# Performance work log

Hardware: AMD Instinct MI355X
Metric: run time of the kernel (lower is better)

## Reference

```python
import jax, jax.numpy as jnp
import numpy as np

# ROUTER_CONFIG constants
TOP_K = 2
EXPLORATION_BONUS = 0.1
EMA_ALPHA = 0.99
B, D, E, O, CTX = 16384, 256, 8, 128, 32


def setup_inputs() -> dict:
    key = jax.random.key(0)
    ks = jax.random.split(key, 16)
    s = 0.05  # small init scale to avoid tanh saturation
    return {
        "x": jax.random.normal(ks[0], (B, D), jnp.float32),
        "targets": jax.random.normal(ks[1], (B, O), jnp.float32),
        "W1": jax.random.normal(ks[2], (D, 64), jnp.float32) * s,
        "b1": jnp.zeros((64,), jnp.float32),
        "W2": jax.random.normal(ks[3], (64, CTX), jnp.float32) * s,
        "b2": jnp.zeros((CTX,), jnp.float32),
        "S1": jax.random.normal(ks[4], (CTX, 32), jnp.float32) * s,
        "sb1": jnp.zeros((32,), jnp.float32),
        "S2": jax.random.normal(ks[5], (32, E), jnp.float32) * s,
        "sb2": jnp.zeros((E,), jnp.float32),
        "We": jax.random.normal(ks[6], (E, D, O), jnp.float32) * s,
        "be": jnp.zeros((E, O), jnp.float32),
        "expert_rewards": jax.random.normal(ks[7], (E,), jnp.float32),
        "routing_ema": jnp.ones((E,), jnp.float32) / E,
        "expert_pulls": jax.random.randint(ks[8], (E,), 0, 500, jnp.int32),
        "total_selections": 1000,
    }


def reference(x, targets, W1, b1, W2, b2, S1, sb1, S2, sb2, We, be,
              expert_rewards, routing_ema, expert_pulls, total_selections):
    # --- context encoder (dropout inactive / eval) ---
    h = jax.nn.relu(x @ W1 + b1)
    context = jnp.tanh(h @ W2 + b2)                      # [B, CTX]
    # --- expert scorer ---
    scores = jax.nn.relu(context @ S1 + sb1) @ S2 + sb2  # [B, E]
    # --- UCB terms ---
    pulls_f = expert_pulls.astype(jnp.float32)
    safe_pulls = jnp.clip(pulls_f, 1.0, None)
    explo = EXPLORATION_BONUS * jnp.sqrt(
        jnp.log(jnp.float32(total_selections)) / safe_pulls)   # [E]
    avg_reward = jnp.where(pulls_f > 0, expert_rewards / safe_pulls, 0.0)
    ucb = scores + avg_reward[None, :] + explo[None, :]   # [B, E]
    # --- top-k selection + routing weights ---
    top_vals, top_idx = jax.lax.top_k(ucb, TOP_K)         # [B, k]
    routing_w = jax.nn.softmax(top_vals, axis=1)          # [B, k]
    # --- expert forward (all experts, then gather selected) ---
    all_out = jnp.einsum('bd,edo->beo', x, We) + be       # [B, E, O]
    sel_out = jnp.take_along_axis(all_out, top_idx[:, :, None], axis=1)  # [B,k,O]
    predictions = jnp.einsum('bk,bko->bo', routing_w, sel_out)           # [B,O]
    # --- per-expert MSE losses -> rewards ---
    losses = jnp.mean((sel_out - targets[:, None, :]) ** 2, axis=-1)  # [B,k]
    rewards = -losses
    # --- vectorized bandit stat updates (replaces python loops) ---
    flat_idx = top_idx.reshape(-1)
    counts = jax.ops.segment_sum(jnp.ones_like(rewards).reshape(-1), flat_idx, num_segments=E)
    rsum = jax.ops.segment_sum(rewards.reshape(-1), flat_idx, num_segments=E)
    new_pulls = pulls_f + counts
    new_total_rewards = expert_rewards + rsum
    new_avg_reward = jnp.where(new_pulls > 0, new_total_rewards / jnp.clip(new_pulls, 1.0, None), 0.0)
    # --- routing-prob EMA update ---
    current_probs = jax.ops.segment_sum(routing_w.reshape(-1), flat_idx, num_segments=E) / x.shape[0]
    new_ema = EMA_ALPHA * routing_ema + (1.0 - EMA_ALPHA) * current_probs
    return predictions, routing_w, top_idx, new_pulls, new_avg_reward, new_ema
```

## Files before the change

kernel.cpp:

```cpp
#include <hip/hip_runtime.h>
#include <math.h>

#define B_SZ   16384
#define D_DIM  256
#define E_NUM  8
#define O_DIM  128
#define CTXW   32
#define H1     64

#define OFF_RW   2097152
#define OFF_IDX  2129920
#define OFF_NP   2162688
#define OFF_NA   2162696
#define OFF_NE   2162704

#define WS_STATS 256
#define WS_LIST  2048

__global__ __launch_bounds__(256) void zero_k(float* out, float* ws) {
    int idx = blockIdx.x * 256 + threadIdx.x;
    if (idx < 524288) ((float4*)out)[idx] = make_float4(0.f, 0.f, 0.f, 0.f);
    if (idx < 512)    ((float4*)ws)[idx]  = make_float4(0.f, 0.f, 0.f, 0.f);
}

__global__ __launch_bounds__(256) void score_k(
    const float* __restrict__ x,
    const float* __restrict__ W1, const float* __restrict__ b1,
    const float* __restrict__ W2, const float* __restrict__ b2,
    const float* __restrict__ S1, const float* __restrict__ sb1,
    const float* __restrict__ S2, const float* __restrict__ sb2,
    const float* __restrict__ er, const int* __restrict__ pulls,
    const int* __restrict__ tsel,
    float* __restrict__ out, int* __restrict__ wsi)
{
    __shared__ float  xs[32][D_DIM];
    __shared__ double hs[32][H1];
    __shared__ double cs[32][CTXW];
    __shared__ double tss[32][CTXW];
    __shared__ double ucb[32][E_NUM];
    __shared__ int    se[64];

    const int t = threadIdx.x, lane = t & 63, wv = t >> 6;
    const int row0 = blockIdx.x * 32;

    const float4* xsrc = (const float4*)(x + (size_t)row0 * D_DIM);
    #pragma unroll
    for (int i = 0; i < 8; ++i)
        ((float4*)xs)[t + i * 256] = xsrc[t + i * 256];
    __syncthreads();

    const int rb = wv * 8;
    {
        double acc0[8], acc1[8];
        double binit = (double)b1[lane];
        #pragma unroll
        for (int r = 0; r < 8; ++r) { acc0[r] = binit; acc1[r] = 0.0; }
        #pragma unroll 4
        for (int d = 0; d < D_DIM; d += 2) {
            double wa = (double)W1[d * H1 + lane];
            double wb = (double)W1[(d + 1) * H1 + lane];
            #pragma unroll
            for (int r = 0; r < 8; ++r) {
                float2 p = *(const float2*)&xs[rb + r][d];
                acc0[r] = fma((double)p.x, wa, acc0[r]);
                acc1[r] = fma((double)p.y, wb, acc1[r]);
            }
        }
        #pragma unroll
        for (int r = 0; r < 8; ++r) {
            double h = acc0[r] + acc1[r];
            hs[rb + r][lane] = h > 0.0 ? h : 0.0;
        }
    }
    __syncthreads();

    {
        const int unit = lane & 31, half = lane >> 5;
        const int ra = rb + half * 4;
        double c0 = (double)b2[unit], c1 = c0, c2 = c0, c3 = c0;
        #pragma unroll 4
        for (int k = 0; k < H1; ++k) {
            double w2v = (double)W2[k * CTXW + unit];
            c0 = fma(hs[ra + 0][k], w2v, c0);
            c1 = fma(hs[ra + 1][k], w2v, c1);
            c2 = fma(hs[ra + 2][k], w2v, c2);
            c3 = fma(hs[ra + 3][k], w2v, c3);
        }
        cs[ra + 0][unit] = tanh(c0);
        cs[ra + 1][unit] = tanh(c1);
        cs[ra + 2][unit] = tanh(c2);
        cs[ra + 3][unit] = tanh(c3);
    }
    __syncthreads();

    {
        const int unit = lane & 31, half = lane >> 5;
        const int ra = rb + half * 4;
        double a0 = (double)sb1[unit], a1 = a0, a2 = a0, a3 = a0;
        #pragma unroll 4
        for (int k = 0; k < CTXW; ++k) {
            double s1v = (double)S1[k * CTXW + unit];
            a0 = fma(cs[ra + 0][k], s1v, a0);
            a1 = fma(cs[ra + 1][k], s1v, a1);
            a2 = fma(cs[ra + 2][k], s1v, a2);
            a3 = fma(cs[ra + 3][k], s1v, a3);
        }
        tss[ra + 0][unit] = a0 > 0.0 ? a0 : 0.0;
        tss[ra + 1][unit] = a1 > 0.0 ? a1 : 0.0;
        tss[ra + 2][unit] = a2 > 0.0 ? a2 : 0.0;
        tss[ra + 3][unit] = a3 > 0.0 ? a3 : 0.0;
    }
    __syncthreads();

    {
        const int e = t & 7, r = t >> 3;
        double a = (double)sb2[e];
        #pragma unroll 4
        for (int k = 0; k < CTXW; ++k)
            a = fma(tss[r][k], (double)S2[k * E_NUM + e], a);
        double pf = (double)pulls[e];
        double sp = pf < 1.0 ? 1.0 : pf;
        double explo = 0.1 * sqrt(log((double)(*tsel)) / sp);
        double avg = pf > 0.0 ? (double)er[e] / sp : 0.0;
        ucb[r][e] = a + avg + explo;
    }
    __syncthreads();

    if (t < 32) {
        double u[E_NUM];
        #pragma unroll
        for (int e = 0; e < E_NUM; ++e) u[e] = ucb[t][e];
        int i0 = 0; double v0 = u[0];
        #pragma unroll
        for (int e = 1; e < E_NUM; ++e) if (u[e] > v0) { v0 = u[e]; i0 = e; }
        int i1 = -1; double v1 = -1.0e300;
        #pragma unroll
        for (int e = 0; e < E_NUM; ++e) {
            if (e == i0) continue;
            if (u[e] > v1) { v1 = u[e]; i1 = e; }
        }
        double exd = exp(v1 - v0);
        double w0 = 1.0 / (1.0 + exd), w1 = exd / (1.0 + exd);
        int row = row0 + t;
        out[OFF_RW  + row * 2]     = (float)w0;
        out[OFF_RW  + row * 2 + 1] = (float)w1;
        out[OFF_IDX + row * 2]     = (float)i0;
        out[OFF_IDX + row * 2 + 1] = (float)i1;
        se[t * 2]     = i0;
        se[t * 2 + 1] = i1;
    }
    __syncthreads();

    if (t < E_NUM) {
        int cntl = 0;
        #pragma unroll
        for (int j = 0; j < 64; ++j) cntl += (se[j] == t);
        if (cntl) {
            int base = atomicAdd(&wsi[t], cntl);
            int k = 0;
            for (int j = 0; j < 64; ++j)
                if (se[j] == t)
                    wsi[WS_LIST + t * B_SZ + base + (k++)] = (row0 + (j >> 1)) * 2 + (j & 1);
        }
    }
}

__global__ __launch_bounds__(256) void expert_k(
    const float* __restrict__ x, const float* __restrict__ tgt,
    const float* __restrict__ We, const float* __restrict__ be,
    float* out, int* __restrict__ wsi, float* __restrict__ wsf)
{
    const int e = blockIdx.x >> 9, chunk = blockIdx.x & 511;
    const int cnt = wsi[e];
    const int base = chunk * 32;
    if (base >= cnt) return;

    __shared__ float xsl[32][68];
    __shared__ float wes[64][O_DIM];
    __shared__ int   rowid[32];
    __shared__ float wsl[32];
    __shared__ float be_sh[O_DIM];

    const int t = threadIdx.x;
    if (t < 32) {
        int en = (base + t < cnt) ? wsi[WS_LIST + e * B_SZ + base + t] : -1;
        rowid[t] = (en >= 0) ? (en >> 1) : -1;
        wsl[t]   = (en >= 0) ? out[OFF_RW + en] : 0.f;
    }
    if (t < O_DIM) be_sh[t] = be[e * O_DIM + t];

    float acc[4][4];
    #pragma unroll
    for (int r = 0; r < 4; ++r)
        #pragma unroll
        for (int j = 0; j < 4; ++j) acc[r][j] = 0.f;

    const int tx = t & 31, ty = t >> 5;
    const int o4 = tx * 4;

    for (int k0 = 0; k0 < 4; ++k0) {
        __syncthreads();
        const float4* wsrc = (const float4*)(We + ((size_t)e * D_DIM + k0 * 64) * O_DIM);
        #pragma unroll
        for (int i = 0; i < 8; ++i)
            ((float4*)wes)[t + i * 256] = wsrc[t + i * 256];
        {
            int r = t >> 3, seg = t & 7;
            int rr = rowid[r] < 0 ? 0 : rowid[r];
            const float* xsr = x + (size_t)rr * D_DIM + k0 * 64 + seg * 8;
            *(float4*)&xsl[r][seg * 8]     = *(const float4*)(xsr);
            *(float4*)&xsl[r][seg * 8 + 4] = *(const float4*)(xsr + 4);
        }
        __syncthreads();
        #pragma unroll 4
        for (int kq = 0; kq < 16; ++kq) {
            float4 w0 = *(float4*)&wes[kq * 4 + 0][o4];
            float4 w1 = *(float4*)&wes[kq * 4 + 1][o4];
            float4 w2 = *(float4*)&wes[kq * 4 + 2][o4];
            float4 w3 = *(float4*)&wes[kq * 4 + 3][o4];
            #pragma unroll
            for (int r = 0; r < 4; ++r) {
                float4 xv = *(float4*)&xsl[ty * 4 + r][kq * 4];
                acc[r][0] = fmaf(xv.x, w0.x, acc[r][0]);
                acc[r][1] = fmaf(xv.x, w0.y, acc[r][1]);
                acc[r][2] = fmaf(xv.x, w0.z, acc[r][2]);
                acc[r][3] = fmaf(xv.x, w0.w, acc[r][3]);
                acc[r][0] = fmaf(xv.y, w1.x, acc[r][0]);
                acc[r][1] = fmaf(xv.y, w1.y, acc[r][1]);
                acc[r][2] = fmaf(xv.y, w1.z, acc[r][2]);
                acc[r][3] = fmaf(xv.y, w1.w, acc[r][3]);
                acc[r][0] = fmaf(xv.z, w2.x, acc[r][0]);
                acc[r][1] = fmaf(xv.z, w2.y, acc[r][1]);
                acc[r][2] = fmaf(xv.z, w2.z, acc[r][2]);
                acc[r][3] = fmaf(xv.z, w2.w, acc[r][3]);
                acc[r][0] = fmaf(xv.w, w3.x, acc[r][0]);
                acc[r][1] = fmaf(xv.w, w3.y, acc[r][1]);
                acc[r][2] = fmaf(xv.w, w3.z, acc[r][2]);
                acc[r][3] = fmaf(xv.w, w3.w, acc[r][3]);
            }
        }
    }

    float cntl = 0.f, rsl = 0.f, wsuml = 0.f;
    #pragma unroll
    for (int r = 0; r < 4; ++r) {
        int li = ty * 4 + r;
        int row = rowid[li];
        bool valid = row >= 0;
        float w = wsl[li];
        float4 tg = make_float4(0.f, 0.f, 0.f, 0.f);
        if (valid) tg = *(const float4*)(tgt + (size_t)row * O_DIM + o4);
        float cf0 = acc[r][0] + be_sh[o4 + 0];
        float cf1 = acc[r][1] + be_sh[o4 + 1];
        float cf2 = acc[r][2] + be_sh[o4 + 2];
        float cf3 = acc[r][3] + be_sh[o4 + 3];
        float d0 = cf0 - tg.x, d1 = cf1 - tg.y, d2 = cf2 - tg.z, d3 = cf3 - tg.w;
        float lpr = d0 * d0 + d1 * d1 + d2 * d2 + d3 * d3;
        if (valid) {
            float* pr = out + (size_t)row * O_DIM + o4;
            atomicAdd(pr + 0, w * cf0);
            atomicAdd(pr + 1, w * cf1);
            atomicAdd(pr + 2, w * cf2);
            atomicAdd(pr + 3, w * cf3);
        }
        #pragma unroll
        for (int off = 1; off < 32; off <<= 1)
            lpr += __shfl_xor(lpr, off, 64);
        if (tx == 0 && valid) {
            cntl += 1.f;
            rsl  += -(lpr * (1.0f / 128.0f));
            wsuml += w;
        }
    }
    if (tx == 0) {
        int cp = WS_STATS + (blockIdx.x & 63) * 24;
        if (cntl > 0.f) {
            atomicAdd(&wsf[cp + e], cntl);
            atomicAdd(&wsf[cp + 8 + e], rsl);
            atomicAdd(&wsf[cp + 16 + e], wsuml);
        }
    }
}

__global__ void final_k(const float* __restrict__ er,
                        const float* __restrict__ ema,
                        const int* __restrict__ pulls,
                        const float* __restrict__ wsf,
                        float* __restrict__ out)
{
    int e = threadIdx.x;
    if (e < E_NUM) {
        double c = 0.0, rs = 0.0, wsum = 0.0;
        for (int cp = 0; cp < 64; ++cp) {
            c    += (double)wsf[WS_STATS + cp * 24 + e];
            rs   += (double)wsf[WS_STATS + cp * 24 + 8 + e];
            wsum += (double)wsf[WS_STATS + cp * 24 + 16 + e];
        }
        double pf = (double)pulls[e];
        double npl = pf + c;
        double ntr = (double)er[e] + rs;
        double sp = npl < 1.0 ? 1.0 : npl;
        double navg = npl > 0.0 ? ntr / sp : 0.0;
        double prob = wsum / (double)B_SZ;
        double nema = 0.99 * (double)ema[e] + 0.01 * prob;
        out[OFF_NP + e] = (float)npl;
        out[OFF_NA + e] = (float)navg;
        out[OFF_NE + e] = (float)nema;
    }
}

extern "C" void kernel_launch(void* const* d_in, const int* in_sizes, int n_in,
                              void* d_out, int out_size, void* d_ws, size_t ws_size,
                              hipStream_t stream) {
    const float* x    = (const float*)d_in[0];
    const float* tgt  = (const float*)d_in[1];
    const float* W1   = (const float*)d_in[2];
    const float* b1   = (const float*)d_in[3];
    const float* W2   = (const float*)d_in[4];
    const float* b2   = (const float*)d_in[5];
    const float* S1   = (const float*)d_in[6];
    const float* sb1  = (const float*)d_in[7];
    const float* S2   = (const float*)d_in[8];
    const float* sb2  = (const float*)d_in[9];
    const float* We   = (const float*)d_in[10];
    const float* be   = (const float*)d_in[11];
    const float* erw  = (const float*)d_in[12];
    const float* ema  = (const float*)d_in[13];
    const int*   pulls = (const int*)d_in[14];
    const int*   tsel  = (const int*)d_in[15];
    float* out = (float*)d_out;
    float* wsf = (float*)d_ws;
    int*   wsi = (int*)d_ws;

    zero_k<<<2048, 256, 0, stream>>>(out, wsf);
    score_k<<<B_SZ / 32, 256, 0, stream>>>(
        x, W1, b1, W2, b2, S1, sb1, S2, sb2, erw, pulls, tsel, out, wsi);
    expert_k<<<E_NUM * 512, 256, 0, stream>>>(x, tgt, We, be, out, wsi, wsf);
    final_k<<<1, 64, 0, stream>>>(erw, ema, pulls, wsf, out);
}
```

Before: 220.9 us.

## Split expert pass by top-k slot to replace atomics with plain stores

New measurement: 194.9 us. 1.13x faster.

```diff
diff --git a/kernel.cpp b/kernel.cpp
--- a/kernel.cpp
+++ b/kernel.cpp
@@ -17,10 +17,9 @@
 #define WS_STATS 256
 #define WS_LIST  2048
 
-__global__ __launch_bounds__(256) void zero_k(float* out, float* ws) {
-    int idx = blockIdx.x * 256 + threadIdx.x;
-    if (idx < 524288) ((float4*)out)[idx] = make_float4(0.f, 0.f, 0.f, 0.f);
-    if (idx < 512)    ((float4*)ws)[idx]  = make_float4(0.f, 0.f, 0.f, 0.f);
+__global__ __launch_bounds__(256) void zero_k(float* ws) {
+    ((float4*)ws)[threadIdx.x]       = make_float4(0.f, 0.f, 0.f, 0.f);
+    ((float4*)ws)[threadIdx.x + 256] = make_float4(0.f, 0.f, 0.f, 0.f);
 }
 
 __global__ __launch_bounds__(256) void score_k(
@@ -151,27 +150,34 @@
     }
     __syncthreads();
 
-    if (t < E_NUM) {
+    if (t < 16) {
+        const int e = t & 7, slot = t >> 3;
         int cntl = 0;
-        #pragma unroll
-        for (int j = 0; j < 64; ++j) cntl += (se[j] == t);
+        for (int j = slot; j < 64; j += 2) cntl += (se[j] == e);
         if (cntl) {
-            int base = atomicAdd(&wsi[t], cntl);
+            int base = atomicAdd(&wsi[slot * 8 + e], cntl);
             int k = 0;
-            for (int j = 0; j < 64; ++j)
-                if (se[j] == t)
-                    wsi[WS_LIST + t * B_SZ + base + (k++)] = (row0 + (j >> 1)) * 2 + (j & 1);
-        }
-    }
-}
-
+            if (slot == 0) {
+                for (int j = 0; j < 64; j += 2)
+                    if (se[j] == e)
+                        wsi[WS_LIST + e * B_SZ + base + (k++)] = row0 + (j >> 1);
+            } else {
+                for (int j = 1; j < 64; j += 2)
+                    if (se[j] == e)
+                        wsi[WS_LIST + e * B_SZ + (B_SZ - 1 - base - (k++))] = row0 + (j >> 1);
+            }
+        }
+    }
+}
+
+template <int SLOT>
 __global__ __launch_bounds__(256) void expert_k(
     const float* __restrict__ x, const float* __restrict__ tgt,
     const float* __restrict__ We, const float* __restrict__ be,
     float* out, int* __restrict__ wsi, float* __restrict__ wsf)
 {
     const int e = blockIdx.x >> 9, chunk = blockIdx.x & 511;
-    const int cnt = wsi[e];
+    const int cnt = wsi[SLOT * 8 + e];
     const int base = chunk * 32;
     if (base >= cnt) return;
 
@@ -183,9 +189,14 @@
 
     const int t = threadIdx.x;
     if (t < 32) {
-        int en = (base + t < cnt) ? wsi[WS_LIST + e * B_SZ + base + t] : -1;
-        rowid[t] = (en >= 0) ? (en >> 1) : -1;
-        wsl[t]   = (en >= 0) ? out[OFF_RW + en] : 0.f;
+        bool ok = (base + t) < cnt;
+        int row = -1;
+        if (ok) {
+            int idx = (SLOT == 0) ? (base + t) : (B_SZ - 1 - (base + t));
+            row = wsi[WS_LIST + e * B_SZ + idx];
+        }
+        rowid[t] = row;
+        wsl[t]   = ok ? out[OFF_RW + row * 2 + SLOT] : 0.f;
     }
     if (t < O_DIM) be_sh[t] = be[e * O_DIM + t];
 
@@ -258,10 +269,14 @@
         float lpr = d0 * d0 + d1 * d1 + d2 * d2 + d3 * d3;
         if (valid) {
             float* pr = out + (size_t)row * O_DIM + o4;
-            atomicAdd(pr + 0, w * cf0);
-            atomicAdd(pr + 1, w * cf1);
-            atomicAdd(pr + 2, w * cf2);
-            atomicAdd(pr + 3, w * cf3);
+            if (SLOT == 0) {
+                float4 v = make_float4(w * cf0, w * cf1, w * cf2, w * cf3);
+                *(float4*)pr = v;
+            } else {
+                float4 p = *(const float4*)pr;
+                p.x += w * cf0; p.y += w * cf1; p.z += w * cf2; p.w += w * cf3;
+                *(float4*)pr = p;
+            }
         }
         #pragma unroll
         for (int off = 1; off < 32; off <<= 1)
@@ -332,9 +347,10 @@
     float* wsf = (float*)d_ws;
     int*   wsi = (int*)d_ws;
 
-    zero_k<<<2048, 256, 0, stream>>>(out, wsf);
+    zero_k<<<1, 256, 0, stream>>>(wsf);
     score_k<<<B_SZ / 32, 256, 0, stream>>>(
         x, W1, b1, W2, b2, S1, sb1, S2, sb2, erw, pulls, tsel, out, wsi);
-    expert_k<<<E_NUM * 512, 256, 0, stream>>>(x, tgt, We, be, out, wsi, wsf);
+    expert_k<0><<<E_NUM * 512, 256, 0, stream>>>(x, tgt, We, be, out, wsi, wsf);
+    expert_k<1><<<E_NUM * 512, 256, 0, stream>>>(x, tgt, We, be, out, wsi, wsf);
     final_k<<<1, 64, 0, stream>>>(erw, ema, pulls, wsf, out);
 }
```
